# Optimization experiments

Measured on AMD Instinct MI355X. Metric: run time of the kernel, lower is better.

## Reference

```python
import jax, jax.numpy as jnp
import numpy as np

B, T, S, E, H, F = 4, 1024, 1024, 512, 8, 2048
D = E // H  # head_dim = 64
SCALE = D ** -0.5
EPS = 1e-5


def setup_inputs() -> dict:
    key = jax.random.key(0)
    ks = jax.random.split(key, 16)
    w = lambda k, shape: jax.random.normal(k, shape, jnp.float32) * 0.02
    inp = {
        'tgt': jax.random.normal(ks[0], (B, T, E), jnp.float32),
        'memory': jax.random.normal(ks[1], (B, S, E), jnp.float32),
    }
    for i, n in enumerate(['sWq', 'sWk', 'sWv', 'sWo', 'cWq', 'cWk', 'cWv', 'cWo']):
        inp[n] = w(ks[2 + i], (E, E))
    for n in ['sbq', 'sbk', 'sbv', 'sbo', 'cbq', 'cbk', 'cbv', 'cbo']:
        inp[n] = jnp.zeros((E,), jnp.float32)
    inp['fW1'] = w(ks[10], (E, F)); inp['fb1'] = jnp.zeros((F,), jnp.float32)
    inp['fW2'] = w(ks[11], (F, E)); inp['fb2'] = jnp.zeros((E,), jnp.float32)
    for n in ['g1', 'g2', 'g3']:
        inp[n] = jnp.ones((E,), jnp.float32)
    for n in ['be1', 'be2', 'be3']:
        inp[n] = jnp.zeros((E,), jnp.float32)
    return inp


def _ln(x, g, b):
    mu = jnp.mean(x, axis=-1, keepdims=True)
    var = jnp.mean(jnp.square(x - mu), axis=-1, keepdims=True)
    return (x - mu) * jax.lax.rsqrt(var + EPS) * g + b


def _mha(xq, xkv, Wq, bq, Wk, bk, Wv, bv, Wo, bo):
    # dense-equivalent of full N^2 edge-list attention (softmax over source nodes per target)
    Bq, Tq, _ = xq.shape
    Skv = xkv.shape[1]
    q = (xq @ Wq + bq).reshape(Bq, Tq, H, D)
    k = (xkv @ Wk + bk).reshape(Bq, Skv, H, D)
    v = (xkv @ Wv + bv).reshape(Bq, Skv, H, D)
    scores = jnp.einsum('bthd,bshd->bhts', q, k) * SCALE
    wts = jax.nn.softmax(scores, axis=-1)
    out = jnp.einsum('bhts,bshd->bthd', wts, v).reshape(Bq, Tq, E)
    return out @ Wo + bo


def reference(tgt, memory,
              sWq, sbq, sWk, sbk, sWv, sbv, sWo, sbo,
              cWq, cbq, cWk, cbk, cWv, cbv, cWo, cbo,
              fW1, fb1, fW2, fb2,
              g1, be1, g2, be2, g3, be3):
    # post-norm decoder layer: self-attn -> cross-attn -> FFN (dropout=0 eval)
    x = _ln(tgt + _mha(tgt, tgt, sWq, sbq, sWk, sbk, sWv, sbv, sWo, sbo), g1, be1)
    x = _ln(x + _mha(x, memory, cWq, cbq, cWk, cbk, cWv, cbv, cWo, cbo), g2, be2)
    ff = jax.nn.relu(x @ fW1 + fb1) @ fW2 + fb2
    x = _ln(x + ff, g3, be3)
    return x
```

## Files before the change

### kernel.cpp

```cpp
#include <hip/hip_runtime.h>

typedef unsigned short ushort_t;
typedef short short8 __attribute__((ext_vector_type(8)));
typedef float float4v __attribute__((ext_vector_type(4)));

__device__ __forceinline__ float bf2f(ushort_t u) {
    union { unsigned int i; float f; } x; x.i = ((unsigned int)u) << 16; return x.f;
}
__device__ __forceinline__ ushort_t f2bf(float f) {
    unsigned int u = __float_as_uint(f);
    unsigned int r = (u + 0x7FFFu + ((u >> 16) & 1u)) >> 16;
    return (ushort_t)r;
}
__device__ __forceinline__ void store_out(float* p, float v) { *p = v; }
__device__ __forceinline__ void store_out(ushort_t* p, float v) { *p = f2bf(v); }

__device__ __forceinline__ void gll16(const ushort_t* g, ushort_t* l) {
    __builtin_amdgcn_global_load_lds(
        (const __attribute__((address_space(1))) void*)g,
        (__attribute__((address_space(3))) void*)l, 16, 0, 0);
}

__global__ void detect_dtype(const ushort_t* __restrict__ tgt, int* __restrict__ flag) {
    __shared__ int red[256];
    const int tid = threadIdx.x;
    int p = 0;
    for (int i = tid; i < 512; i += 256) {
        ushort_t u = tgt[i];
        int e = (u >> 7) & 0xFF;
        if (u == 0 || (e >= 100 && e <= 140)) ++p;
    }
    red[tid] = p; __syncthreads();
    for (int off = 128; off > 0; off >>= 1) {
        if (tid < off) red[tid] += red[tid + off];
        __syncthreads();
    }
    if (tid == 0) flag[0] = (red[0] >= 480) ? 1 : 0;
}

__global__ __launch_bounds__(256) void prep_all(
    const void* sWq, const void* sWk, const void* sWv, const void* sWo,
    const void* cWq, const void* cWk, const void* cWv, const void* cWo,
    const void* fW1, const void* fW2,
    const void* tgt, const void* mem,
    const void* sbq, const void* sbk, const void* sbv, const void* sbo,
    const void* cbq, const void* cbk, const void* cbv, const void* cbo,
    const void* fb1, const void* fb2,
    ushort_t* __restrict__ wb, ushort_t* __restrict__ tb, ushort_t* __restrict__ mb,
    float* __restrict__ pb, const int* __restrict__ dflag)
{
    const bool f32 = (dflag[0] == 0);
    const int tid = threadIdx.x;
    const int z = blockIdx.z;

    if (z < 10) {
        const void* src; ushort_t* dst; int Kd, Nd;
        switch (z) {
            case 0: src = sWq; dst = wb + 0;       Kd = 512;  Nd = 512;  break;
            case 1: src = sWk; dst = wb + 262144;  Kd = 512;  Nd = 512;  break;
            case 2: src = sWv; dst = wb + 524288;  Kd = 512;  Nd = 512;  break;
            case 3: src = sWo; dst = wb + 786432;  Kd = 512;  Nd = 512;  break;
            case 4: src = cWq; dst = wb + 1048576; Kd = 512;  Nd = 512;  break;
            case 5: src = cWk; dst = wb + 1310720; Kd = 512;  Nd = 512;  break;
            case 6: src = cWv; dst = wb + 1572864; Kd = 512;  Nd = 512;  break;
            case 7: src = cWo; dst = wb + 1835008; Kd = 512;  Nd = 512;  break;
            case 8: src = fW1; dst = wb + 2097152; Kd = 512;  Nd = 2048; break;
            default:src = fW2; dst = wb + 3145728; Kd = 2048; Nd = 512;  break;
        }
        const int k0 = blockIdx.x * 64, n0 = blockIdx.y * 64;
        if (k0 >= Kd || n0 >= Nd) return;
        __shared__ ushort_t T[64][65];
#pragma unroll
        for (int i = 0; i < 16; ++i) {
            int j = i * 256 + tid;
            int r = j >> 6, c = j & 63;
            float v = f32 ? ((const float*)src)[(size_t)(k0 + r) * Nd + n0 + c]
                          : bf2f(((const ushort_t*)src)[(size_t)(k0 + r) * Nd + n0 + c]);
            T[r][c] = f2bf(v);
        }
        __syncthreads();
#pragma unroll
        for (int i = 0; i < 16; ++i) {
            int j = i * 256 + tid;
            int n = j >> 6, k = j & 63;
            dst[(size_t)(n0 + n) * Kd + k0 + k] = T[k][n];
        }
        return;
    }

    const int bid = blockIdx.x * 32 + blockIdx.y;
    if (z < 12) {
        const void* src = (z == 10) ? tgt : mem;
        ushort_t* dst = (z == 10) ? tb : mb;
        const int i = (bid * 256 + tid) * 8;
        if (f32) {
            float4 v0 = *(const float4*)((const float*)src + i);
            float4 v1 = *(const float4*)((const float*)src + i + 4);
            ushort_t o[8] = { f2bf(v0.x), f2bf(v0.y), f2bf(v0.z), f2bf(v0.w),
                              f2bf(v1.x), f2bf(v1.y), f2bf(v1.z), f2bf(v1.w) };
            *(uint4*)(dst + i) = *(const uint4*)o;
        } else {
            *(uint4*)(dst + i) = *(const uint4*)((const ushort_t*)src + i);
        }
        return;
    }

    {
        const int i = bid * 256 + tid;
        if (bid >= 26 || i >= 6656) return;
        const void* src; int off;
        if      (i < 512)  { src = sbq; off = i; }
        else if (i < 1024) { src = sbk; off = i - 512; }
        else if (i < 1536) { src = sbv; off = i - 1024; }
        else if (i < 2048) { src = sbo; off = i - 1536; }
        else if (i < 2560) { src = cbq; off = i - 2048; }
        else if (i < 3072) { src = cbk; off = i - 2560; }
        else if (i < 3584) { src = cbv; off = i - 3072; }
        else if (i < 4096) { src = cbo; off = i - 3584; }
        else if (i < 6144) { src = fb1; off = i - 4096; }
        else               { src = fb2; off = i - 6144; }
        pb[i] = f32 ? ((const float*)src)[off] : bf2f(((const ushort_t*)src)[off]);
    }
}

template<typename OutT, bool RELU, int BN>
__global__ __launch_bounds__(256) void gemm_tn(
    const ushort_t* __restrict__ A1, const ushort_t* __restrict__ A2,
    int ySplit, int lda,
    const ushort_t* __restrict__ Wt, int ldw,
    const float* __restrict__ bias,
    OutT* __restrict__ C, int ldc, int K)
{
    constexpr int MI = (BN == 128) ? 4 : 2;
    __shared__ ushort_t As[2][128][32];
    __shared__ ushort_t Bs[2][BN][32];
    const int tid = threadIdx.x;
    const int wave = tid >> 6, lane = tid & 63;
    const int quad = lane >> 4, l16 = lane & 15;
    const int m0 = blockIdx.x * 128, n0 = blockIdx.y * BN;
    const int wm = (BN == 128) ? (wave >> 1) * 64 : wave * 32;
    const int wn = (BN == 128) ? (wave & 1) * 64 : 0;
    const ushort_t* A = (((int)blockIdx.y) < ySplit) ? A1 : A2;

    float4v acc[MI][4];
#pragma unroll
    for (int mi = 0; mi < MI; ++mi)
#pragma unroll
        for (int ni = 0; ni < 4; ++ni) {
            acc[mi][ni][0] = 0.f; acc[mi][ni][1] = 0.f;
            acc[mi][ni][2] = 0.f; acc[mi][ni][3] = 0.f;
        }

    const int srow = lane >> 2;
    const int scc  = lane & 3;
    const int sg   = (scc - (lane >> 3)) & 3;
    const ushort_t* aptr0 = A  + (size_t)(m0 + wave * 16 + srow) * lda + sg * 8;
    const ushort_t* aptr1 = A  + (size_t)(m0 + 64 + wave * 16 + srow) * lda + sg * 8;
    const ushort_t* bptr0 = Wt + (size_t)(n0 + wave * 16 + srow) * ldw + sg * 8;
    const ushort_t* bptr1 = Wt + (size_t)(n0 + 64 + wave * 16 + srow) * ldw + sg * 8;

    gll16(aptr0, &As[0][wave * 16][0]);
    gll16(aptr1, &As[0][64 + wave * 16][0]);
    gll16(bptr0, &Bs[0][wave * 16][0]);
    if (BN == 128) gll16(bptr1, &Bs[0][64 + wave * 16][0]);

    const int ca = ((quad + (l16 >> 1)) & 3) * 8;
    int cur = 0;
    for (int k0 = 0; k0 < K; k0 += 32) {
        __syncthreads();
        if (k0 + 32 < K) {
            const int nb = cur ^ 1, ko = k0 + 32;
            gll16(aptr0 + ko, &As[nb][wave * 16][0]);
            gll16(aptr1 + ko, &As[nb][64 + wave * 16][0]);
            gll16(bptr0 + ko, &Bs[nb][wave * 16][0]);
            if (BN == 128) gll16(bptr1 + ko, &Bs[nb][64 + wave * 16][0]);
        }
        short8 af[MI], bfr[4];
#pragma unroll
        for (int mi = 0; mi < MI; ++mi)
            af[mi] = *(const short8*)(&As[cur][wm + mi * 16 + l16][ca]);
#pragma unroll
        for (int ni = 0; ni < 4; ++ni)
            bfr[ni] = *(const short8*)(&Bs[cur][wn + ni * 16 + l16][ca]);
#pragma unroll
        for (int mi = 0; mi < MI; ++mi)
#pragma unroll
            for (int ni = 0; ni < 4; ++ni)
                acc[mi][ni] = __builtin_amdgcn_mfma_f32_16x16x32_bf16(
                    af[mi], bfr[ni], acc[mi][ni], 0, 0, 0);
        cur ^= 1;
    }

#pragma unroll
    for (int ni = 0; ni < 4; ++ni) {
        const int col = n0 + wn + ni * 16 + l16;
        const float bv = bias[col];
#pragma unroll
        for (int mi = 0; mi < MI; ++mi)
#pragma unroll
            for (int r = 0; r < 4; ++r) {
                const int row = m0 + wm + mi * 16 + quad * 4 + r;
                float v = acc[mi][ni][r] + bv;
                if (RELU) v = fmaxf(v, 0.f);
                store_out(&C[(size_t)row * ldc + col], v);
            }
    }
}

__global__ __launch_bounds__(256) void attn_mfma(ushort_t* __restrict__ QKV)
{
    const int S = 1536;
    __shared__ ushort_t Qs[64][72];
    __shared__ ushort_t Ks[64][72];
    __shared__ ushort_t Vt[64][72];

    const int tid  = threadIdx.x;
    const int wave = tid >> 6, lane = tid & 63;
    const int quad = lane >> 4, l16 = lane & 15;
    const int qt = blockIdx.x, bh = blockIdx.y;
    const int b = bh >> 3, h = bh & 7;
    const size_t rowQ = (size_t)b * 1024 + qt * 64;
    const size_t kv0  = (size_t)b * 1024;

    const int kr = tid >> 2, kc = (tid & 3) * 16;
    const int sp = tid >> 3, dc = (tid & 7) * 8;
    const int vr0 = sp * 2;
    const int vrg = vr0 >> 3, vrof = vr0 & 7;

    {
        const ushort_t* src = QKV + (rowQ + kr) * S + h * 64 + kc;
        *(uint4*)(&Qs[kr][kc])     = *(const uint4*)(src);
        *(uint4*)(&Qs[kr][kc + 8]) = *(const uint4*)(src + 8);
    }
    __syncthreads();
    short8 qf[2];
    qf[0] = *(const short8*)(&Qs[wave * 16 + l16][quad * 8]);
    qf[1] = *(const short8*)(&Qs[wave * 16 + l16][32 + quad * 8]);
    ushort_t (* __restrict__ Ps)[72] = Qs;

    const float CEXP = 0.125f * 1.44269504f;
    const float MREF = 16.0f * CEXP;
    float lsum[4];
    float4v oacc[4];
#pragma unroll
    for (int r = 0; r < 4; ++r) lsum[r] = 0.f;
#pragma unroll
    for (int n = 0; n < 4; ++n) { oacc[n][0]=0.f; oacc[n][1]=0.f; oacc[n][2]=0.f; oacc[n][3]=0.f; }

    uint4 kA, kB, vA, vB;
    {
        const ushort_t* ksrc = QKV + (kv0 + kr) * S + 512 + h * 64 + kc;
        kA = *(const uint4*)(ksrc);
        kB = *(const uint4*)(ksrc + 8);
        const ushort_t* vsrc = QKV + (kv0 + vr0) * S + 1024 + h * 64 + dc;
        vA = *(const uint4*)(vsrc);
        vB = *(const uint4*)(vsrc + S);
    }

    for (int s0 = 0; s0 < 1024; s0 += 64) {
        __syncthreads();
        *(uint4*)(&Ks[kr][kc])     = kA;
        *(uint4*)(&Ks[kr][kc + 8]) = kB;
        {
            const ushort_t* ae = (const ushort_t*)&vA;
            const ushort_t* be = (const ushort_t*)&vB;
#pragma unroll
            for (int j = 0; j < 8; ++j) {
                const int d = dc + j;
                const int cc = (vrg ^ (d >> 4)) & 7;
                *(unsigned int*)(&Vt[d][cc * 8 + vrof]) =
                    (unsigned int)ae[j] | ((unsigned int)be[j] << 16);
            }
        }
        __syncthreads();
        if (s0 + 64 < 1024) {
            const ushort_t* ksrc = QKV + (kv0 + s0 + 64 + kr) * S + 512 + h * 64 + kc;
            kA = *(const uint4*)(ksrc);
            kB = *(const uint4*)(ksrc + 8);
            const ushort_t* vsrc = QKV + (kv0 + s0 + 64 + vr0) * S + 1024 + h * 64 + dc;
            vA = *(const uint4*)(vsrc);
            vB = *(const uint4*)(vsrc + S);
        }

        float4v sc[4];
#pragma unroll
        for (int sb = 0; sb < 4; ++sb) {
            float4v z; z[0]=0.f; z[1]=0.f; z[2]=0.f; z[3]=0.f;
            short8 kf0 = *(const short8*)(&Ks[sb * 16 + l16][quad * 8]);
            short8 kf1 = *(const short8*)(&Ks[sb * 16 + l16][32 + quad * 8]);
            z = __builtin_amdgcn_mfma_f32_16x16x32_bf16(qf[0], kf0, z, 0, 0, 0);
            z = __builtin_amdgcn_mfma_f32_16x16x32_bf16(qf[1], kf1, z, 0, 0, 0);
            sc[sb] = z;
        }

#pragma unroll
        for (int sb = 0; sb < 4; ++sb)
#pragma unroll
            for (int r = 0; r < 4; ++r) {
                float p = exp2f(fmaf(sc[sb][r], CEXP, -MREF));
                lsum[r] += p;
                Ps[wave * 16 + quad * 4 + r][sb * 16 + l16] = f2bf(p);
            }

        short8 pf[2];
        pf[0] = *(const short8*)(&Ps[wave * 16 + l16][quad * 8]);
        pf[1] = *(const short8*)(&Ps[wave * 16 + l16][32 + quad * 8]);
#pragma unroll
        for (int n = 0; n < 4; ++n) {
#pragma unroll
            for (int kc2 = 0; kc2 < 2; ++kc2) {
                const int cc = ((kc2 * 4 + quad) ^ n) & 7;
                short8 vf = *(const short8*)(&Vt[n * 16 + l16][cc * 8]);
                oacc[n] = __builtin_amdgcn_mfma_f32_16x16x32_bf16(pf[kc2], vf, oacc[n], 0, 0, 0);
            }
        }
    }

#pragma unroll
    for (int msk = 1; msk < 16; msk <<= 1)
#pragma unroll
        for (int r = 0; r < 4; ++r) lsum[r] += __shfl_xor(lsum[r], msk);
    float inv[4];
#pragma unroll
    for (int r = 0; r < 4; ++r) inv[r] = 1.f / lsum[r];
#pragma unroll
    for (int n = 0; n < 4; ++n)
#pragma unroll
        for (int r = 0; r < 4; ++r) {
            const size_t row = rowQ + wave * 16 + quad * 4 + r;
            QKV[row * S + h * 64 + n * 16 + l16] = f2bf(oacc[n][r] * inv[r]);
        }
}

template<bool RES_EXT, bool DELTA_F32, bool OUT_FLAG>
__global__ __launch_bounds__(256) void ln_kernel(
    const void* __restrict__ res, const void* __restrict__ delta,
    const void* __restrict__ g, const void* __restrict__ be,
    void* __restrict__ out, const int* __restrict__ dflag)
{
    const int E = 512;
    const bool extf32 = (dflag[0] == 0);
    const int row = blockIdx.x, tid = threadIdx.x;
    const int wave = tid >> 6, lane = tid & 63;
    const size_t base = (size_t)row * E;
    const int i0 = tid, i1 = tid + 256;

    float r0, r1;
    if (RES_EXT && extf32) {
        r0 = ((const float*)res)[base + i0];
        r1 = ((const float*)res)[base + i1];
    } else {
        r0 = bf2f(((const ushort_t*)res)[base + i0]);
        r1 = bf2f(((const ushort_t*)res)[base + i1]);
    }
    float d0v, d1v;
    if (DELTA_F32) {
        d0v = ((const float*)delta)[base + i0];
        d1v = ((const float*)delta)[base + i1];
    } else {
        d0v = bf2f(((const ushort_t*)delta)[base + i0]);
        d1v = bf2f(((const ushort_t*)delta)[base + i1]);
    }
    float x0 = r0 + d0v, x1 = r1 + d1v;

    __shared__ float red8[8];
    float s = x0 + x1;
#pragma unroll
    for (int m = 1; m < 64; m <<= 1) s += __shfl_xor(s, m);
    if (lane == 0) red8[wave] = s;
    __syncthreads();
    float mean = (red8[0] + red8[1] + red8[2] + red8[3]) * (1.0f / 512.0f);
    float dd0 = x0 - mean, dd1 = x1 - mean;
    float v = dd0 * dd0 + dd1 * dd1;
#pragma unroll
    for (int m = 1; m < 64; m <<= 1) v += __shfl_xor(v, m);
    if (lane == 0) red8[4 + wave] = v;
    __syncthreads();
    float rstd = rsqrtf((red8[4] + red8[5] + red8[6] + red8[7]) * (1.0f / 512.0f) + 1e-5f);

    float g0, g1v, b0, b1;
    if (extf32) {
        g0 = ((const float*)g)[i0];  g1v = ((const float*)g)[i1];
        b0 = ((const float*)be)[i0]; b1  = ((const float*)be)[i1];
    } else {
        g0 = bf2f(((const ushort_t*)g)[i0]);  g1v = bf2f(((const ushort_t*)g)[i1]);
        b0 = bf2f(((const ushort_t*)be)[i0]); b1  = bf2f(((const ushort_t*)be)[i1]);
    }
    float y0 = dd0 * rstd * g0 + b0;
    float y1 = dd1 * rstd * g1v + b1;
    if (OUT_FLAG && extf32) {
        ((float*)out)[base + i0] = y0; ((float*)out)[base + i1] = y1;
    } else {
        ((ushort_t*)out)[base + i0] = f2bf(y0);
        ((ushort_t*)out)[base + i1] = f2bf(y1);
    }
}


extern "C" void kernel_launch(void* const* d_in, const int* in_sizes, int n_in,
                              void* d_out, int out_size, void* d_ws, size_t ws_size,
                              hipStream_t stream) {
    const void* tgt = d_in[0];
    const void* mem = d_in[1];
    const void* sWq = d_in[2];  const void* sWk = d_in[3];
    const void* sWv = d_in[4];  const void* sWo = d_in[5];
    const void* cWq = d_in[6];  const void* cWk = d_in[7];
    const void* cWv = d_in[8];  const void* cWo = d_in[9];
    const void* sbq = d_in[10]; const void* sbk = d_in[11];
    const void* sbv = d_in[12]; const void* sbo = d_in[13];
    const void* cbq = d_in[14]; const void* cbk = d_in[15];
    const void* cbv = d_in[16]; const void* cbo = d_in[17];
    const void* fW1 = d_in[18]; const void* fb1 = d_in[19];
    const void* fW2 = d_in[20]; const void* fb2 = d_in[21];
    const void* g1  = d_in[22]; const void* g2  = d_in[23];
    const void* g3  = d_in[24];
    const void* be1 = d_in[25]; const void* be2 = d_in[26];
    const void* be3 = d_in[27];

    char* ws = (char*)d_ws;
    const size_t MB = 1048576;
    ushort_t* qkv = (ushort_t*)(ws + 0 * MB);
    ushort_t* hb  = (ushort_t*)(ws + 0 * MB);
    ushort_t* po  = (ushort_t*)(ws + 12 * MB);
    ushort_t* xb  = (ushort_t*)(ws + 16 * MB);
    ushort_t* tb  = (ushort_t*)(ws + 20 * MB);
    ushort_t* mb  = (ushort_t*)(ws + 24 * MB);
    float*    of  = (float*)   (ws + 20 * MB);
    ushort_t* wb  = (ushort_t*)(ws + 28 * MB);
    float*    pb  = (float*)   (ws + 36 * MB);
    int*   dflag  = (int*)     (ws + 36 * MB + 262144);

    const ushort_t* sWqkv_t = wb + 0;
    const ushort_t* sWo_t   = wb + 786432;
    const ushort_t* cWqkv_t = wb + 1048576;
    const ushort_t* cWo_t   = wb + 1835008;
    const ushort_t* fW1_t   = wb + 2097152;
    const ushort_t* fW2_t   = wb + 3145728;

    dim3 blk(256);

    detect_dtype<<<dim3(1), blk, 0, stream>>>((const ushort_t*)tgt, dflag);
    prep_all<<<dim3(32, 32, 13), blk, 0, stream>>>(
        sWq, sWk, sWv, sWo, cWq, cWk, cWv, cWo, fW1, fW2,
        tgt, mem, sbq, sbk, sbv, sbo, cbq, cbk, cbv, cbo, fb1, fb2,
        wb, tb, mb, pb, dflag);

    dim3 gattn(16, 32);

    gemm_tn<ushort_t, false, 128><<<dim3(32, 12), blk, 0, stream>>>(tb, tb, 0, 512, sWqkv_t, 512, pb + 0, qkv, 1536, 512);
    attn_mfma<<<gattn, blk, 0, stream>>>(qkv);
    gemm_tn<ushort_t, false, 64><<<dim3(32, 8), blk, 0, stream>>>(qkv, qkv, 0, 1536, sWo_t, 512, pb + 1536, po, 512, 512);
    ln_kernel<true, false, false><<<dim3(4096), blk, 0, stream>>>(tgt, po, g1, be1, xb, dflag);

    gemm_tn<ushort_t, false, 128><<<dim3(32, 12), blk, 0, stream>>>(xb, mb, 4, 512, cWqkv_t, 512, pb + 2048, qkv, 1536, 512);
    attn_mfma<<<gattn, blk, 0, stream>>>(qkv);
    gemm_tn<ushort_t, false, 64><<<dim3(32, 8), blk, 0, stream>>>(qkv, qkv, 0, 1536, cWo_t, 512, pb + 3584, po, 512, 512);
    ln_kernel<false, false, false><<<dim3(4096), blk, 0, stream>>>(xb, po, g2, be2, xb, dflag);

    gemm_tn<ushort_t, true, 128><<<dim3(32, 16), blk, 0, stream>>>(xb, xb, 0, 512, fW1_t, 512, pb + 4096, hb, 2048, 512);
    gemm_tn<float, false, 64><<<dim3(32, 8), blk, 0, stream>>>(hb, hb, 0, 2048, fW2_t, 2048, pb + 6144, of, 512, 2048);
    ln_kernel<false, true, true><<<dim3(4096), blk, 0, stream>>>(xb, of, g3, be3, d_out, dflag);
}
```

Baseline: 305.5 us.

## Split attention KV loop across two wave groups with LDS reduction

```diff
diff --git a/kernel.cpp b/kernel.cpp
--- a/kernel.cpp
+++ b/kernel.cpp
@@ -207,36 +207,40 @@
     }
 }
 
-__global__ __launch_bounds__(256) void attn_mfma(ushort_t* __restrict__ QKV)
+__global__ __launch_bounds__(512) void attn_mfma(ushort_t* __restrict__ QKV)
 {
     const int S = 1536;
-    __shared__ ushort_t Qs[64][72];
-    __shared__ ushort_t Ks[64][72];
-    __shared__ ushort_t Vt[64][72];
+    __shared__ ushort_t PsA[64][72];
+    __shared__ ushort_t PsB[64][72];
+    __shared__ ushort_t Ks[2][64][72];
+    __shared__ ushort_t Vt[2][64][72];
 
     const int tid  = threadIdx.x;
-    const int wave = tid >> 6, lane = tid & 63;
+    const int w    = tid >> 6;
+    const int g    = w >> 2;
+    const int wq   = w & 3;
+    const int lane = tid & 63;
     const int quad = lane >> 4, l16 = lane & 15;
+    const int ht   = tid & 255;
     const int qt = blockIdx.x, bh = blockIdx.y;
     const int b = bh >> 3, h = bh & 7;
     const size_t rowQ = (size_t)b * 1024 + qt * 64;
     const size_t kv0  = (size_t)b * 1024;
 
-    const int kr = tid >> 2, kc = (tid & 3) * 16;
-    const int sp = tid >> 3, dc = (tid & 7) * 8;
+    const int kr = ht >> 2, kc = (ht & 3) * 16;
+    const int sp = ht >> 3, dc = (ht & 7) * 8;
     const int vr0 = sp * 2;
     const int vrg = vr0 >> 3, vrof = vr0 & 7;
 
     {
-        const ushort_t* src = QKV + (rowQ + kr) * S + h * 64 + kc;
-        *(uint4*)(&Qs[kr][kc])     = *(const uint4*)(src);
-        *(uint4*)(&Qs[kr][kc + 8]) = *(const uint4*)(src + 8);
+        const int r = tid >> 3, c = (tid & 7) * 8;
+        *(uint4*)(&PsA[r][c]) = *(const uint4*)(QKV + (rowQ + r) * S + h * 64 + c);
     }
     __syncthreads();
     short8 qf[2];
-    qf[0] = *(const short8*)(&Qs[wave * 16 + l16][quad * 8]);
-    qf[1] = *(const short8*)(&Qs[wave * 16 + l16][32 + quad * 8]);
-    ushort_t (* __restrict__ Ps)[72] = Qs;
+    qf[0] = *(const short8*)(&PsA[wq * 16 + l16][quad * 8]);
+    qf[1] = *(const short8*)(&PsA[wq * 16 + l16][32 + quad * 8]);
+    ushort_t (* __restrict__ Ps)[72] = g ? PsB : PsA;
 
     const float CEXP = 0.125f * 1.44269504f;
     const float MREF = 16.0f * CEXP;
@@ -249,18 +253,19 @@
 
     uint4 kA, kB, vA, vB;
     {
-        const ushort_t* ksrc = QKV + (kv0 + kr) * S + 512 + h * 64 + kc;
+        const size_t sr = kv0 + g * 64;
+        const ushort_t* ksrc = QKV + (sr + kr) * S + 512 + h * 64 + kc;
         kA = *(const uint4*)(ksrc);
         kB = *(const uint4*)(ksrc + 8);
-        const ushort_t* vsrc = QKV + (kv0 + vr0) * S + 1024 + h * 64 + dc;
+        const ushort_t* vsrc = QKV + (sr + vr0) * S + 1024 + h * 64 + dc;
         vA = *(const uint4*)(vsrc);
         vB = *(const uint4*)(vsrc + S);
     }
 
-    for (int s0 = 0; s0 < 1024; s0 += 64) {
+    for (int it = 0; it < 8; ++it) {
         __syncthreads();
-        *(uint4*)(&Ks[kr][kc])     = kA;
-        *(uint4*)(&Ks[kr][kc + 8]) = kB;
+        *(uint4*)(&Ks[g][kr][kc])     = kA;
+        *(uint4*)(&Ks[g][kr][kc + 8]) = kB;
         {
             const ushort_t* ae = (const ushort_t*)&vA;
             const ushort_t* be = (const ushort_t*)&vB;
@@ -268,16 +273,17 @@
             for (int j = 0; j < 8; ++j) {
                 const int d = dc + j;
                 const int cc = (vrg ^ (d >> 4)) & 7;
-                *(unsigned int*)(&Vt[d][cc * 8 + vrof]) =
+                *(unsigned int*)(&Vt[g][d][cc * 8 + vrof]) =
                     (unsigned int)ae[j] | ((unsigned int)be[j] << 16);
             }
         }
         __syncthreads();
-        if (s0 + 64 < 1024) {
-            const ushort_t* ksrc = QKV + (kv0 + s0 + 64 + kr) * S + 512 + h * 64 + kc;
+        if (it < 7) {
+            const size_t sr = kv0 + (it + 1) * 128 + g * 64;
+            const ushort_t* ksrc = QKV + (sr + kr) * S + 512 + h * 64 + kc;
             kA = *(const uint4*)(ksrc);
             kB = *(const uint4*)(ksrc + 8);
-            const ushort_t* vsrc = QKV + (kv0 + s0 + 64 + vr0) * S + 1024 + h * 64 + dc;
+            const ushort_t* vsrc = QKV + (sr + vr0) * S + 1024 + h * 64 + dc;
             vA = *(const uint4*)(vsrc);
             vB = *(const uint4*)(vsrc + S);
         }
@@ -286,8 +292,8 @@
 #pragma unroll
         for (int sb = 0; sb < 4; ++sb) {
             float4v z; z[0]=0.f; z[1]=0.f; z[2]=0.f; z[3]=0.f;
-            short8 kf0 = *(const short8*)(&Ks[sb * 16 + l16][quad * 8]);
-            short8 kf1 = *(const short8*)(&Ks[sb * 16 + l16][32 + quad * 8]);
+            short8 kf0 = *(const short8*)(&Ks[g][sb * 16 + l16][quad * 8]);
+            short8 kf1 = *(const short8*)(&Ks[g][sb * 16 + l16][32 + quad * 8]);
             z = __builtin_amdgcn_mfma_f32_16x16x32_bf16(qf[0], kf0, z, 0, 0, 0);
             z = __builtin_amdgcn_mfma_f32_16x16x32_bf16(qf[1], kf1, z, 0, 0, 0);
             sc[sb] = z;
@@ -299,18 +305,18 @@
             for (int r = 0; r < 4; ++r) {
                 float p = exp2f(fmaf(sc[sb][r], CEXP, -MREF));
                 lsum[r] += p;
-                Ps[wave * 16 + quad * 4 + r][sb * 16 + l16] = f2bf(p);
+                Ps[wq * 16 + quad * 4 + r][sb * 16 + l16] = f2bf(p);
             }
 
         short8 pf[2];
-        pf[0] = *(const short8*)(&Ps[wave * 16 + l16][quad * 8]);
-        pf[1] = *(const short8*)(&Ps[wave * 16 + l16][32 + quad * 8]);
+        pf[0] = *(const short8*)(&Ps[wq * 16 + l16][quad * 8]);
+        pf[1] = *(const short8*)(&Ps[wq * 16 + l16][32 + quad * 8]);
 #pragma unroll
         for (int n = 0; n < 4; ++n) {
 #pragma unroll
             for (int kc2 = 0; kc2 < 2; ++kc2) {
                 const int cc = ((kc2 * 4 + quad) ^ n) & 7;
-                short8 vf = *(const short8*)(&Vt[n * 16 + l16][cc * 8]);
+                short8 vf = *(const short8*)(&Vt[g][n * 16 + l16][cc * 8]);
                 oacc[n] = __builtin_amdgcn_mfma_f32_16x16x32_bf16(pf[kc2], vf, oacc[n], 0, 0, 0);
             }
         }
@@ -320,16 +326,36 @@
     for (int msk = 1; msk < 16; msk <<= 1)
 #pragma unroll
         for (int r = 0; r < 4; ++r) lsum[r] += __shfl_xor(lsum[r], msk);
-    float inv[4];
-#pragma unroll
-    for (int r = 0; r < 4; ++r) inv[r] = 1.f / lsum[r];
-#pragma unroll
-    for (int n = 0; n < 4; ++n)
-#pragma unroll
-        for (int r = 0; r < 4; ++r) {
-            const size_t row = rowQ + wave * 16 + quad * 4 + r;
-            QKV[row * S + h * 64 + n * 16 + l16] = f2bf(oacc[n][r] * inv[r]);
-        }
+
+    float* exch = (float*)&Ks[0][0][0];
+    float* exl  = (float*)&Vt[0][0][0];
+    __syncthreads();
+    if (g == 1) {
+#pragma unroll
+        for (int n = 0; n < 4; ++n)
+#pragma unroll
+            for (int r = 0; r < 4; ++r)
+                exch[((wq * 4 + n) * 4 + r) * 64 + lane] = oacc[n][r];
+        if (l16 == 0)
+#pragma unroll
+            for (int r = 0; r < 4; ++r) exl[wq * 16 + quad * 4 + r] = lsum[r];
+    }
+    __syncthreads();
+    if (g == 0) {
+#pragma unroll
+        for (int r = 0; r < 4; ++r) lsum[r] += exl[wq * 16 + quad * 4 + r];
+        float inv[4];
+#pragma unroll
+        for (int r = 0; r < 4; ++r) inv[r] = 1.f / lsum[r];
+#pragma unroll
+        for (int n = 0; n < 4; ++n)
+#pragma unroll
+            for (int r = 0; r < 4; ++r) {
+                float o = oacc[n][r] + exch[((wq * 4 + n) * 4 + r) * 64 + lane];
+                const size_t row = rowQ + wq * 16 + quad * 4 + r;
+                QKV[row * S + h * 64 + n * 16 + l16] = f2bf(o * inv[r]);
+            }
+    }
 }
 
 template<bool RES_EXT, bool DELTA_F32, bool OUT_FLAG>
@@ -446,14 +472,15 @@
         wb, tb, mb, pb, dflag);
 
     dim3 gattn(16, 32);
+    dim3 blk512(512);
 
     gemm_tn<ushort_t, false, 128><<<dim3(32, 12), blk, 0, stream>>>(tb, tb, 0, 512, sWqkv_t, 512, pb + 0, qkv, 1536, 512);
-    attn_mfma<<<gattn, blk, 0, stream>>>(qkv);
+    attn_mfma<<<gattn, blk512, 0, stream>>>(qkv);
     gemm_tn<ushort_t, false, 64><<<dim3(32, 8), blk, 0, stream>>>(qkv, qkv, 0, 1536, sWo_t, 512, pb + 1536, po, 512, 512);
     ln_kernel<true, false, false><<<dim3(4096), blk, 0, stream>>>(tgt, po, g1, be1, xb, dflag);
 
     gemm_tn<ushort_t, false, 128><<<dim3(32, 12), blk, 0, stream>>>(xb, mb, 4, 512, cWqkv_t, 512, pb + 2048, qkv, 1536, 512);
-    attn_mfma<<<gattn, blk, 0, stream>>>(qkv);
+    attn_mfma<<<gattn, blk512, 0, stream>>>(qkv);
     gemm_tn<ushort_t, false, 64><<<dim3(32, 8), blk, 0, stream>>>(qkv, qkv, 0, 1536, cWo_t, 512, pb + 3584, po, 512, 512);
     ln_kernel<false, false, false><<<dim3(4096), blk, 0, stream>>>(xb, po, g2, be2, xb, dflag);
 
```

Result: faster. 299.3 us (-2.0%).
